# Optimization experiments

Measured on AMD Instinct MI355X. Metric: run time of the kernel, lower is better.

Reference implementation:

```python
import jax, jax.numpy as jnp
import numpy as np

D_MODEL = 1024
NUM_HEADS = 16
HEAD_DIM = D_MODEL // NUM_HEADS
LN_EPS = 1e-3  # keras LayerNormalization default epsilon


def setup_inputs() -> dict:
    key = jax.random.key(0)
    ks = jax.random.split(key, 10)
    B, T = 2, 2048
    s = 1.0 / np.sqrt(D_MODEL)
    return {
        "x": jax.random.normal(ks[0], (B, T, D_MODEL), dtype=jnp.float32),
        "Wq": jax.random.normal(ks[1], (D_MODEL, D_MODEL), dtype=jnp.float32) * s,
        "Wk": jax.random.normal(ks[2], (D_MODEL, D_MODEL), dtype=jnp.float32) * s,
        "Wv": jax.random.normal(ks[3], (D_MODEL, D_MODEL), dtype=jnp.float32) * s,
        "Wg": jax.random.normal(ks[4], (D_MODEL, D_MODEL), dtype=jnp.float32) * s,
        "bg": jnp.zeros((D_MODEL,), dtype=jnp.float32),
        "Wo": jax.random.normal(ks[5], (D_MODEL, D_MODEL), dtype=jnp.float32) * s,
        "bo": jnp.zeros((D_MODEL,), dtype=jnp.float32),
        "ln_gamma": jnp.ones((D_MODEL,), dtype=jnp.float32),
        "ln_beta": jnp.zeros((D_MODEL,), dtype=jnp.float32),
    }


def reference(x, Wq, Wk, Wv, Wg, bg, Wo, bo, ln_gamma, ln_beta):
    B, T, D = x.shape
    H, dh = NUM_HEADS, HEAD_DIM

    def split_heads(z):
        return z.reshape(B, T, H, dh).transpose(0, 2, 1, 3)  # [B,H,T,dh]

    Q = split_heads(x @ Wq)
    K = split_heads(x @ Wk)
    V = split_heads(x @ Wv)
    G = jax.nn.swish(x @ Wg + bg)  # [B,T,D]

    # Per-head causal decay mask D[h,m,n] = gamma_h^(m-n) for m>=n else 0
    idx = jnp.arange(T, dtype=jnp.float32)
    diff = idx[:, None] - idx[None, :]  # [T,T]
    causal = (diff >= 0).astype(jnp.float32)
    gammas = 1.0 - 2.0 ** (-5.0 - jnp.arange(H, dtype=jnp.float32))  # [H]
    Dmask = (gammas[:, None, None] ** jnp.maximum(diff, 0.0)) * causal  # [H,T,T]

    scale = float(dh) ** 0.5
    scores = jnp.einsum('bhtd,bhsd->bhts', Q, K) / scale  # [B,H,T,T]
    ret = jnp.einsum('bhts,bhsd->bhtd', scores * Dmask[None], V)  # [B,H,T,dh]
    ret = ret.transpose(0, 2, 1, 3).reshape(B, T, D)  # concat heads

    # LayerNorm (axis=-1, keras default eps=1e-3)
    mu = jnp.mean(ret, axis=-1, keepdims=True)
    var = jnp.mean(jnp.square(ret - mu), axis=-1, keepdims=True)
    ln = (ret - mu) / jnp.sqrt(var + LN_EPS) * ln_gamma + ln_beta

    return (ln * G) @ Wo + bo
```

## Files before the change

kernel.cpp:

```cpp
#include <hip/hip_runtime.h>

#define D_MODEL 1024
#define NHEADS  16
#define HDIM    64
#define BATCH   2
#define SEQ     2048
#define ROWS    (BATCH*SEQ)
#define CHUNK   128
#define NCHUNK  (SEQ/CHUNK)
#define LN_EPS  1e-3f

typedef unsigned short ushort_t;
typedef __attribute__((ext_vector_type(4))) float          f32x4;
typedef __attribute__((ext_vector_type(8))) short          s16x8;
typedef __attribute__((ext_vector_type(4))) unsigned short u16x4;
typedef __attribute__((ext_vector_type(8))) unsigned short u16x8;

__device__ __forceinline__ ushort_t f2b(float f) {
    union { float f; unsigned int u; } v; v.f = f;
    unsigned int r = v.u + 0x7fffu + ((v.u >> 16) & 1u);
    return (ushort_t)(r >> 16);
}
__device__ __forceinline__ float b2f(ushort_t b) {
    union { unsigned int u; float f; } v; v.u = ((unsigned int)b) << 16;
    return v.f;
}

__global__ __launch_bounds__(256) void cast_x_kernel(const float* __restrict__ x,
                                                     ushort_t* __restrict__ xb) {
    int idx = (blockIdx.x * 256 + threadIdx.x) * 4;
    f32x4 v = *(const f32x4*)(x + idx);
    u16x4 o;
    o.x = f2b(v.x); o.y = f2b(v.y); o.z = f2b(v.z); o.w = f2b(v.w);
    *(u16x4*)(xb + idx) = o;
}

__global__ __launch_bounds__(256) void wt_transpose_kernel(
        const float* __restrict__ Wq, const float* __restrict__ Wk,
        const float* __restrict__ Wv, const float* __restrict__ Wg,
        const float* __restrict__ Wo,
        ushort_t* __restrict__ WcatT, ushort_t* __restrict__ WoT) {
    __shared__ float tile[32][33];
    int z = blockIdx.z;
    const float* W = (z == 0) ? Wq : (z == 1) ? Wk : (z == 2) ? Wv : (z == 3) ? Wg : Wo;
    ushort_t* dst = (z < 4) ? (WcatT + (size_t)z * 1024 * 1024) : WoT;
    int n0 = blockIdx.x * 32, k0 = blockIdx.y * 32;
    int tx = threadIdx.x, ty = threadIdx.y;
#pragma unroll
    for (int i = 0; i < 4; i++) {
        int k = k0 + ty + i * 8;
        tile[ty + i * 8][tx] = W[(size_t)k * 1024 + n0 + tx];
    }
    __syncthreads();
#pragma unroll
    for (int i = 0; i < 4; i++) {
        int n = n0 + ty + i * 8;
        dst[(size_t)n * 1024 + k0 + tx] = f2b(tile[tx][ty + i * 8]);
    }
}

#define LDW 72
__global__ __launch_bounds__(256, 2) void gemm_kernel(
        const ushort_t* __restrict__ A, const ushort_t* __restrict__ BT,
        int K, int N, int mode, const float* __restrict__ bias,
        ushort_t* __restrict__ Yout, float* __restrict__ Fout) {
    extern __shared__ char smem[];
    ushort_t* As = (ushort_t*)smem;
    ushort_t* Bs = As + 128 * LDW;
    int t = threadIdx.x;
    int row0 = blockIdx.y * 128, col0 = blockIdx.x * 128;
    int w = t >> 6, lane = t & 63;
    int wr = (w >> 1) * 64, wc = (w & 1) * 64;
    int qd = lane >> 4, ln = lane & 15;

    f32x4 acc[4][4];
#pragma unroll
    for (int i = 0; i < 4; i++)
#pragma unroll
        for (int j = 0; j < 4; j++) acc[i][j] = (f32x4)0.0f;

    for (int k0 = 0; k0 < K; k0 += 64) {
#pragma unroll
        for (int g = t; g < 1024; g += 256) {
            int r = g >> 3, kg = (g & 7) << 3;
            *(u16x8*)(As + r * LDW + kg) =
                *(const u16x8*)(A + (size_t)(row0 + r) * K + k0 + kg);
            *(u16x8*)(Bs + r * LDW + kg) =
                *(const u16x8*)(BT + (size_t)(col0 + r) * K + k0 + kg);
        }
        __syncthreads();
#pragma unroll
        for (int kk = 0; kk < 64; kk += 32) {
            s16x8 af[4], bf[4];
#pragma unroll
            for (int i = 0; i < 4; i++)
                af[i] = *(const s16x8*)(As + (wr + i * 16 + ln) * LDW + kk + qd * 8);
#pragma unroll
            for (int j = 0; j < 4; j++)
                bf[j] = *(const s16x8*)(Bs + (wc + j * 16 + ln) * LDW + kk + qd * 8);
#pragma unroll
            for (int i = 0; i < 4; i++)
#pragma unroll
                for (int j = 0; j < 4; j++)
                    acc[i][j] = __builtin_amdgcn_mfma_f32_16x16x32_bf16(
                        af[i], bf[j], acc[i][j], 0, 0, 0);
        }
        __syncthreads();
    }

#pragma unroll
    for (int i = 0; i < 4; i++)
#pragma unroll
        for (int j = 0; j < 4; j++) {
            int n = col0 + wc + j * 16 + ln;
#pragma unroll
            for (int r = 0; r < 4; r++) {
                int m = row0 + wr + i * 16 + qd * 4 + r;
                float v = acc[i][j][r];
                if (mode == 0) {
                    int region = n >> 10;
                    if (region == 0) v *= 0.125f;
                    else if (region == 3) {
                        v += bias[n & 1023];
                        v = v / (1.0f + __expf(-v));
                    }
                    Yout[(size_t)m * N + n] = f2b(v);
                } else {
                    Fout[(size_t)m * N + n] = v + bias[n];
                }
            }
        }
}

__global__ __launch_bounds__(256) void chunk_states_kernel(const ushort_t* __restrict__ Y,
                                                           float* __restrict__ Astate) {
    __shared__ float Kw[64 * 64];
    __shared__ float Vv[64 * 64];
    int c = blockIdx.x, h = blockIdx.y, b = blockIdx.z;
    int t = threadIdx.x;
    float gamma = 1.0f - exp2f(-5.0f - (float)h);
    float l2g = log2f(gamma);
    int row0 = b * SEQ + c * CHUNK;
    int colK = D_MODEL + h * HDIM;
    int colV = 2 * D_MODEL + h * HDIM;
    int dq = (t & 15) * 4, d1b = t >> 4;

    f32x4 acc[4];
#pragma unroll
    for (int a = 0; a < 4; a++) acc[a] = (f32x4)0.0f;

    for (int half = 0; half < 2; half++) {
        __syncthreads();
        for (int l = t; l < 4096; l += 256) {
            int j = l >> 6, d = l & 63;
            int jj = half * 64 + j;
            size_t row = (size_t)(row0 + jj) * 4096;
            Kw[j * 64 + d] = b2f(Y[row + colK + d]) * exp2f((float)(127 - jj) * l2g);
            Vv[j * 64 + d] = b2f(Y[row + colV + d]);
        }
        __syncthreads();
#pragma unroll 4
        for (int j = 0; j < 64; j++) {
            f32x4 v4 = *(const f32x4*)(Vv + j * 64 + dq);
#pragma unroll
            for (int a = 0; a < 4; a++) {
                float kv = Kw[j * 64 + d1b + 16 * a];
                acc[a] += kv * v4;
            }
        }
    }
    size_t base = ((size_t)((b * NHEADS + h) * NCHUNK + c)) * 4096;
#pragma unroll
    for (int a = 0; a < 4; a++)
        *(f32x4*)(Astate + base + (size_t)(d1b + 16 * a) * 64 + dq) = acc[a];
}

__global__ __launch_bounds__(256) void scan_kernel(const float* __restrict__ Astate,
                                                   float* __restrict__ Sprev) {
    int h = blockIdx.x, b = blockIdx.y;
    int bh = b * NHEADS + h;
    float gamma = 1.0f - exp2f(-5.0f - (float)h);
    float gC = exp2f(128.0f * log2f(gamma));
    for (int g = threadIdx.x; g < 1024; g += 256) {
        f32x4 S = (f32x4)0.0f;
        for (int c = 0; c < NCHUNK; c++) {
            size_t off = ((size_t)bh * NCHUNK + c) * 4096 + g * 4;
            *(f32x4*)(Sprev + off) = S;
            f32x4 Ain = *(const f32x4*)(Astate + off);
            S = S * gC + Ain;
        }
    }
}

#define VT_LDW 136
#define CO_ELEMS (128*LDW*2 + 64*LDW*2 + 64*VT_LDW)
__global__ __launch_bounds__(256, 2) void chunk_out_kernel(const ushort_t* __restrict__ Y,
                                                           const float* __restrict__ Sprev,
                                                           float* __restrict__ ret) {
    extern __shared__ char smem[];
    ushort_t* Qs   = (ushort_t*)smem;
    ushort_t* Kc   = Qs + 128 * LDW;
    ushort_t* Sphi = Kc + 128 * LDW;
    ushort_t* Splo = Sphi + 64 * LDW;
    ushort_t* Vt   = Splo + 64 * LDW;
    ushort_t* Pl   = Qs;

    int c = blockIdx.x, h = blockIdx.y, b = blockIdx.z;
    int t = threadIdx.x;
    float gamma = 1.0f - exp2f(-5.0f - (float)h);
    float l2g = log2f(gamma);
    int row0 = b * SEQ + c * CHUNK;

    for (int g = t; g < 1024; g += 256) {
        int i = g >> 3, dg = (g & 7) * 8;
        size_t src = (size_t)(row0 + i) * 4096 + h * HDIM + dg;
        *(u16x8*)(Qs + i * LDW + dg) = *(const u16x8*)(Y + src);
        *(u16x8*)(Kc + i * LDW + dg) = *(const u16x8*)(Y + src + D_MODEL);
        u16x8 v = *(const u16x8*)(Y + src + 2 * D_MODEL);
#pragma unroll
        for (int k2 = 0; k2 < 8; k2++) Vt[(dg + k2) * VT_LDW + i] = v[k2];
    }
    {
        size_t sbase = ((size_t)((b * NHEADS + h) * NCHUNK + c)) * 4096;
        for (int g = t; g < 1024; g += 256) {
            int e = g >> 4, dg = (g & 15) * 4;
            f32x4 s4 = *(const f32x4*)(Sprev + sbase + e * 64 + dg);
#pragma unroll
            for (int k2 = 0; k2 < 4; k2++) {
                float s = s4[k2];
                ushort_t hb = f2b(s);
                float lo = s - b2f(hb);
                Sphi[(dg + k2) * LDW + e] = hb;
                Splo[(dg + k2) * LDW + e] = f2b(lo);
            }
        }
    }
    __syncthreads();

    int w = t >> 6, lane = t & 63;
    int wr = w * 32;
    int qd = lane >> 4, ln = lane & 15;

    s16x8 aq[2][2];
#pragma unroll
    for (int mt = 0; mt < 2; mt++)
#pragma unroll
        for (int ks = 0; ks < 2; ks++)
            aq[mt][ks] = *(const s16x8*)(Qs + (wr + mt * 16 + ln) * LDW + ks * 32 + qd * 8);

    float prow[2][4], pcolm[8];
#pragma unroll
    for (int mt = 0; mt < 2; mt++)
#pragma unroll
        for (int r = 0; r < 4; r++)
            prow[mt][r] = exp2f((float)(wr + mt * 16 + qd * 4 + r + 1) * l2g);
#pragma unroll
    for (int nt = 0; nt < 8; nt++)
        pcolm[nt] = exp2f(-(float)(nt * 16 + ln + 1) * l2g);

    f32x4 out[2][4];
#pragma unroll
    for (int mt = 0; mt < 2; mt++)
#pragma unroll
        for (int dt = 0; dt < 4; dt++) out[mt][dt] = (f32x4)0.0f;
#pragma unroll
    for (int dt = 0; dt < 4; dt++)
#pragma unroll
        for (int ks = 0; ks < 2; ks++) {
            s16x8 bh_ = *(const s16x8*)(Sphi + (dt * 16 + ln) * LDW + ks * 32 + qd * 8);
            s16x8 bl_ = *(const s16x8*)(Splo + (dt * 16 + ln) * LDW + ks * 32 + qd * 8);
#pragma unroll
            for (int mt = 0; mt < 2; mt++) {
                out[mt][dt] = __builtin_amdgcn_mfma_f32_16x16x32_bf16(
                    aq[mt][ks], bh_, out[mt][dt], 0, 0, 0);
                out[mt][dt] = __builtin_amdgcn_mfma_f32_16x16x32_bf16(
                    aq[mt][ks], bl_, out[mt][dt], 0, 0, 0);
            }
        }
#pragma unroll
    for (int mt = 0; mt < 2; mt++)
#pragma unroll
        for (int dt = 0; dt < 4; dt++)
#pragma unroll
            for (int r = 0; r < 4; r++) out[mt][dt][r] *= prow[mt][r];

    f32x4 sc[2][8];
#pragma unroll
    for (int mt = 0; mt < 2; mt++)
#pragma unroll
        for (int nt = 0; nt < 8; nt++) sc[mt][nt] = (f32x4)0.0f;
#pragma unroll
    for (int nt = 0; nt < 8; nt++)
#pragma unroll
        for (int ks = 0; ks < 2; ks++) {
            s16x8 bk = *(const s16x8*)(Kc + (nt * 16 + ln) * LDW + ks * 32 + qd * 8);
#pragma unroll
            for (int mt = 0; mt < 2; mt++)
                sc[mt][nt] = __builtin_amdgcn_mfma_f32_16x16x32_bf16(
                    aq[mt][ks], bk, sc[mt][nt], 0, 0, 0);
        }
    __syncthreads();

#pragma unroll
    for (int mt = 0; mt < 2; mt++)
#pragma unroll
        for (int nt = 0; nt < 8; nt++) {
            int j = nt * 16 + ln;
#pragma unroll
            for (int r = 0; r < 4; r++) {
                int i = wr + mt * 16 + qd * 4 + r;
                float v = (j <= i) ? sc[mt][nt][r] * (prow[mt][r] * pcolm[nt]) : 0.0f;
                Pl[i * VT_LDW + j] = f2b(v);
            }
        }
    __syncthreads();

#pragma unroll
    for (int ks = 0; ks < 4; ks++) {
        s16x8 ap[2];
#pragma unroll
        for (int mt = 0; mt < 2; mt++)
            ap[mt] = *(const s16x8*)(Pl + (wr + mt * 16 + ln) * VT_LDW + ks * 32 + qd * 8);
#pragma unroll
        for (int dt = 0; dt < 4; dt++) {
            s16x8 bv = *(const s16x8*)(Vt + (dt * 16 + ln) * VT_LDW + ks * 32 + qd * 8);
#pragma unroll
            for (int mt = 0; mt < 2; mt++)
                out[mt][dt] = __builtin_amdgcn_mfma_f32_16x16x32_bf16(
                    ap[mt], bv, out[mt][dt], 0, 0, 0);
        }
    }

#pragma unroll
    for (int mt = 0; mt < 2; mt++)
#pragma unroll
        for (int dt = 0; dt < 4; dt++)
#pragma unroll
            for (int r = 0; r < 4; r++) {
                int i = wr + mt * 16 + qd * 4 + r;
                ret[(size_t)(row0 + i) * D_MODEL + h * HDIM + dt * 16 + ln] = out[mt][dt][r];
            }
}

__global__ __launch_bounds__(256) void ln_gate_kernel(const float* __restrict__ ret,
                                                      const ushort_t* __restrict__ Y,
                                                      const float* __restrict__ lgam,
                                                      const float* __restrict__ lbet,
                                                      ushort_t* __restrict__ LNG) {
    int row = blockIdx.x, t = threadIdx.x;
    f32x4 v = *(const f32x4*)(ret + (size_t)row * D_MODEL + t * 4);
    float s  = v.x + v.y + v.z + v.w;
    float sq = v.x * v.x + v.y * v.y + v.z * v.z + v.w * v.w;
#pragma unroll
    for (int m = 1; m < 64; m <<= 1) {
        s  += __shfl_xor(s, m);
        sq += __shfl_xor(sq, m);
    }
    __shared__ float red[8];
    int w = t >> 6, lane = t & 63;
    if (lane == 0) { red[w * 2] = s; red[w * 2 + 1] = sq; }
    __syncthreads();
    s  = red[0] + red[2] + red[4] + red[6];
    sq = red[1] + red[3] + red[5] + red[7];
    float mu  = s * (1.0f / 1024.0f);
    float var = sq * (1.0f / 1024.0f) - mu * mu;
    float inv = rsqrtf(var + LN_EPS);
    int col = t * 4;
    u16x4 ug = *(const u16x4*)(Y + (size_t)row * 4096 + 3 * D_MODEL + col);
    u16x4 o;
    o.x = f2b(((v.x - mu) * inv * lgam[col + 0] + lbet[col + 0]) * b2f(ug.x));
    o.y = f2b(((v.y - mu) * inv * lgam[col + 1] + lbet[col + 1]) * b2f(ug.y));
    o.z = f2b(((v.z - mu) * inv * lgam[col + 2] + lbet[col + 2]) * b2f(ug.z));
    o.w = f2b(((v.w - mu) * inv * lgam[col + 3] + lbet[col + 3]) * b2f(ug.w));
    *(u16x4*)(LNG + (size_t)row * D_MODEL + col) = o;
}

extern "C" void kernel_launch(void* const* d_in, const int* in_sizes, int n_in,
                              void* d_out, int out_size, void* d_ws, size_t ws_size,
                              hipStream_t stream) {
    const float* x   = (const float*)d_in[0];
    const float* Wq  = (const float*)d_in[1];
    const float* Wk  = (const float*)d_in[2];
    const float* Wv  = (const float*)d_in[3];
    const float* Wg  = (const float*)d_in[4];
    const float* bg  = (const float*)d_in[5];
    const float* Wo  = (const float*)d_in[6];
    const float* bo  = (const float*)d_in[7];
    const float* lng = (const float*)d_in[8];
    const float* lnb = (const float*)d_in[9];
    float* out = (float*)d_out;

    char* ws = (char*)d_ws;
    ushort_t* xb    = (ushort_t*)(ws);
    ushort_t* WcatT = (ushort_t*)(ws + (8ull  << 20));
    ushort_t* WoT   = (ushort_t*)(ws + (16ull << 20));
    ushort_t* Yb    = (ushort_t*)(ws + (18ull << 20));
    float*    retb  = (float*)   (ws + (50ull << 20));
    float*    Ast   = (float*)   (ws + (66ull << 20));
    float*    Sprv  = (float*)   (ws + (74ull << 20));
    ushort_t* LNGb  = (ushort_t*)(ws + (82ull << 20));

    const int CO_BYTES = CO_ELEMS * 2;

    hipFuncSetAttribute(reinterpret_cast<const void*>(gemm_kernel),
                        hipFuncAttributeMaxDynamicSharedMemorySize, 2 * 128 * LDW * 2);
    hipFuncSetAttribute(reinterpret_cast<const void*>(chunk_out_kernel),
                        hipFuncAttributeMaxDynamicSharedMemorySize, CO_BYTES);

    cast_x_kernel<<<ROWS * D_MODEL / 1024, 256, 0, stream>>>(x, xb);
    wt_transpose_kernel<<<dim3(32, 32, 5), dim3(32, 8), 0, stream>>>(
        Wq, Wk, Wv, Wg, Wo, WcatT, WoT);

    gemm_kernel<<<dim3(32, 32), 256, 2 * 128 * LDW * 2, stream>>>(
        xb, WcatT, 1024, 4096, 0, bg, Yb, (float*)nullptr);

    chunk_states_kernel<<<dim3(NCHUNK, NHEADS, BATCH), 256, 0, stream>>>(Yb, Ast);
    scan_kernel<<<dim3(NHEADS, BATCH), 256, 0, stream>>>(Ast, Sprv);
    chunk_out_kernel<<<dim3(NCHUNK, NHEADS, BATCH), 256, CO_BYTES, stream>>>(
        Yb, Sprv, retb);

    ln_gate_kernel<<<ROWS, 256, 0, stream>>>(retb, Yb, lng, lnb, LNGb);

    gemm_kernel<<<dim3(8, 32), 256, 2 * 128 * LDW * 2, stream>>>(
        LNGb, WoT, 1024, 1024, 1, bo, (ushort_t*)nullptr, out);
}
```

Measured before the change: 235.9 us.

## Use async global-to-LDS loads with XOR swizzle in GEMM; MFMA chunk states

The GEMM tile loads now go straight from global memory into LDS through global_load_lds. An XOR-swizzled layout replaces the padded rows, which avoids bank conflicts without the register round-trip. The chunk_states kernel is rewritten to stage the decayed K and V transposed in bf16 and to compute the 64x64 state with MFMA instead of scalar FP32 FMAs. The state accumulation now uses bf16-rounded decayed K, a small precision trade-off. The async-load swizzle assumes each lane writes a contiguous 16-byte slot in LDS.

```diff
diff --git a/kernel.cpp b/kernel.cpp
--- a/kernel.cpp
+++ b/kernel.cpp
@@ -24,6 +24,13 @@
 __device__ __forceinline__ float b2f(ushort_t b) {
     union { unsigned int u; float f; } v; v.u = ((unsigned int)b) << 16;
     return v.f;
+}
+
+__device__ __forceinline__ void async_load16(const ushort_t* g, ushort_t* l) {
+    __builtin_amdgcn_global_load_lds(
+        (const __attribute__((address_space(1))) unsigned int*)(g),
+        (__attribute__((address_space(3))) unsigned int*)(l),
+        16, 0, 0);
 }
 
 __global__ __launch_bounds__(256) void cast_x_kernel(const float* __restrict__ x,
@@ -59,19 +66,19 @@
     }
 }
 
-#define LDW 72
 __global__ __launch_bounds__(256, 2) void gemm_kernel(
         const ushort_t* __restrict__ A, const ushort_t* __restrict__ BT,
         int K, int N, int mode, const float* __restrict__ bias,
         ushort_t* __restrict__ Yout, float* __restrict__ Fout) {
     extern __shared__ char smem[];
     ushort_t* As = (ushort_t*)smem;
-    ushort_t* Bs = As + 128 * LDW;
+    ushort_t* Bs = As + 128 * 64;
     int t = threadIdx.x;
     int row0 = blockIdx.y * 128, col0 = blockIdx.x * 128;
     int w = t >> 6, lane = t & 63;
     int wr = (w >> 1) * 64, wc = (w & 1) * 64;
     int qd = lane >> 4, ln = lane & 15;
+    int lx = ln & 7;
 
     f32x4 acc[4][4];
 #pragma unroll
@@ -81,23 +88,25 @@
 
     for (int k0 = 0; k0 < K; k0 += 64) {
 #pragma unroll
-        for (int g = t; g < 1024; g += 256) {
-            int r = g >> 3, kg = (g & 7) << 3;
-            *(u16x8*)(As + r * LDW + kg) =
-                *(const u16x8*)(A + (size_t)(row0 + r) * K + k0 + kg);
-            *(u16x8*)(Bs + r * LDW + kg) =
-                *(const u16x8*)(BT + (size_t)(col0 + r) * K + k0 + kg);
+        for (int p = 0; p < 4; p++) {
+            int g = p * 256 + t;
+            int r = g >> 3;
+            int kb = g & 7;
+            int kbs = kb ^ (r & 7);
+            async_load16(A + (size_t)(row0 + r) * K + k0 + kbs * 8, As + g * 8);
+            async_load16(BT + (size_t)(col0 + r) * K + k0 + kbs * 8, Bs + g * 8);
         }
         __syncthreads();
 #pragma unroll
         for (int kk = 0; kk < 64; kk += 32) {
             s16x8 af[4], bf[4];
+            int kxa = ((kk >> 3) + qd) ^ lx;
 #pragma unroll
             for (int i = 0; i < 4; i++)
-                af[i] = *(const s16x8*)(As + (wr + i * 16 + ln) * LDW + kk + qd * 8);
+                af[i] = *(const s16x8*)(As + (wr + i * 16 + ln) * 64 + kxa * 8);
 #pragma unroll
             for (int j = 0; j < 4; j++)
-                bf[j] = *(const s16x8*)(Bs + (wc + j * 16 + ln) * LDW + kk + qd * 8);
+                bf[j] = *(const s16x8*)(Bs + (wc + j * 16 + ln) * 64 + kxa * 8);
 #pragma unroll
             for (int i = 0; i < 4; i++)
 #pragma unroll
@@ -132,47 +141,58 @@
         }
 }
 
+#define SJ 136
 __global__ __launch_bounds__(256) void chunk_states_kernel(const ushort_t* __restrict__ Y,
                                                            float* __restrict__ Astate) {
-    __shared__ float Kw[64 * 64];
-    __shared__ float Vv[64 * 64];
+    __shared__ ushort_t Ktd[64 * SJ];
+    __shared__ ushort_t Vtd[64 * SJ];
     int c = blockIdx.x, h = blockIdx.y, b = blockIdx.z;
     int t = threadIdx.x;
     float gamma = 1.0f - exp2f(-5.0f - (float)h);
     float l2g = log2f(gamma);
     int row0 = b * SEQ + c * CHUNK;
     int colK = D_MODEL + h * HDIM;
-    int colV = 2 * D_MODEL + h * HDIM;
-    int dq = (t & 15) * 4, d1b = t >> 4;
+
+    for (int g = t; g < 1024; g += 256) {
+        int j = g >> 3, dg = (g & 7) * 8;
+        size_t src = (size_t)(row0 + j) * 4096 + colK + dg;
+        u16x8 k8 = *(const u16x8*)(Y + src);
+        u16x8 v8 = *(const u16x8*)(Y + src + D_MODEL);
+        float dec = exp2f((float)(127 - j) * l2g);
+#pragma unroll
+        for (int q = 0; q < 8; q++) {
+            Ktd[(dg + q) * SJ + j] = f2b(b2f(k8[q]) * dec);
+            Vtd[(dg + q) * SJ + j] = v8[q];
+        }
+    }
+    __syncthreads();
+
+    int w = t >> 6, lane = t & 63;
+    int wr = w * 16;
+    int qd = lane >> 4, ln = lane & 15;
+
+    s16x8 af[4];
+#pragma unroll
+    for (int ks = 0; ks < 4; ks++)
+        af[ks] = *(const s16x8*)(Ktd + (wr + ln) * SJ + ks * 32 + qd * 8);
 
     f32x4 acc[4];
 #pragma unroll
-    for (int a = 0; a < 4; a++) acc[a] = (f32x4)0.0f;
-
-    for (int half = 0; half < 2; half++) {
-        __syncthreads();
-        for (int l = t; l < 4096; l += 256) {
-            int j = l >> 6, d = l & 63;
-            int jj = half * 64 + j;
-            size_t row = (size_t)(row0 + jj) * 4096;
-            Kw[j * 64 + d] = b2f(Y[row + colK + d]) * exp2f((float)(127 - jj) * l2g);
-            Vv[j * 64 + d] = b2f(Y[row + colV + d]);
-        }
-        __syncthreads();
-#pragma unroll 4
-        for (int j = 0; j < 64; j++) {
-            f32x4 v4 = *(const f32x4*)(Vv + j * 64 + dq);
-#pragma unroll
-            for (int a = 0; a < 4; a++) {
-                float kv = Kw[j * 64 + d1b + 16 * a];
-                acc[a] += kv * v4;
-            }
-        }
-    }
+    for (int nt = 0; nt < 4; nt++) {
+        acc[nt] = (f32x4)0.0f;
+#pragma unroll
+        for (int ks = 0; ks < 4; ks++) {
+            s16x8 bf = *(const s16x8*)(Vtd + (nt * 16 + ln) * SJ + ks * 32 + qd * 8);
+            acc[nt] = __builtin_amdgcn_mfma_f32_16x16x32_bf16(af[ks], bf, acc[nt], 0, 0, 0);
+        }
+    }
+
     size_t base = ((size_t)((b * NHEADS + h) * NCHUNK + c)) * 4096;
 #pragma unroll
-    for (int a = 0; a < 4; a++)
-        *(f32x4*)(Astate + base + (size_t)(d1b + 16 * a) * 64 + dq) = acc[a];
+    for (int nt = 0; nt < 4; nt++)
+#pragma unroll
+        for (int r = 0; r < 4; r++)
+            Astate[base + (size_t)(wr + qd * 4 + r) * 64 + nt * 16 + ln] = acc[nt][r];
 }
 
 __global__ __launch_bounds__(256) void scan_kernel(const float* __restrict__ Astate,
@@ -192,6 +212,7 @@
     }
 }
 
+#define LDW 72
 #define VT_LDW 136
 #define CO_ELEMS (128*LDW*2 + 64*LDW*2 + 64*VT_LDW)
 __global__ __launch_bounds__(256, 2) void chunk_out_kernel(const ushort_t* __restrict__ Y,
@@ -400,10 +421,11 @@
     float*    Sprv  = (float*)   (ws + (74ull << 20));
     ushort_t* LNGb  = (ushort_t*)(ws + (82ull << 20));
 
+    const int GEMM_LDS = 2 * 128 * 64 * 2;
     const int CO_BYTES = CO_ELEMS * 2;
 
     hipFuncSetAttribute(reinterpret_cast<const void*>(gemm_kernel),
-                        hipFuncAttributeMaxDynamicSharedMemorySize, 2 * 128 * LDW * 2);
+                        hipFuncAttributeMaxDynamicSharedMemorySize, GEMM_LDS);
     hipFuncSetAttribute(reinterpret_cast<const void*>(chunk_out_kernel),
                         hipFuncAttributeMaxDynamicSharedMemorySize, CO_BYTES);
 
@@ -411,7 +433,7 @@
     wt_transpose_kernel<<<dim3(32, 32, 5), dim3(32, 8), 0, stream>>>(
         Wq, Wk, Wv, Wg, Wo, WcatT, WoT);
 
-    gemm_kernel<<<dim3(32, 32), 256, 2 * 128 * LDW * 2, stream>>>(
+    gemm_kernel<<<dim3(32, 32), 256, GEMM_LDS, stream>>>(
         xb, WcatT, 1024, 4096, 0, bg, Yb, (float*)nullptr);
 
     chunk_states_kernel<<<dim3(NCHUNK, NHEADS, BATCH), 256, 0, stream>>>(Yb, Ast);
@@ -421,6 +443,6 @@
 
     ln_gate_kernel<<<ROWS, 256, 0, stream>>>(retb, Yb, lng, lnb, LNGb);
 
-    gemm_kernel<<<dim3(8, 32), 256, 2 * 128 * LDW * 2, stream>>>(
+    gemm_kernel<<<dim3(8, 32), 256, GEMM_LDS, stream>>>(
         LNGb, WoT, 1024, 1024, 1, bo, (ushort_t*)nullptr, out);
 }
```

Result: faster. 204.9 us (-13.2%).
